# Optimization experiments

Hardware: AMD Instinct MI355X
Metric: run time of the kernel (lower is better)

The kernel has to match this reference:

```python
import jax, jax.numpy as jnp
import numpy as np

N_NODES = 100_000
N_EDGES = 1_000_000
IN_CH = 32
EDGE_CH = 16
OUT_CH = 32
D_CAT = 2 * IN_CH + EDGE_CH  # 80
D_MID = 56                   # linspace(80, 32, 3)[1]


def setup_inputs() -> dict:
    key = jax.random.key(0)
    ks = jax.random.split(key, 8)
    x = jax.random.normal(ks[0], (N_NODES, IN_CH), dtype=jnp.float32)
    edge_index = jax.random.randint(ks[1], (2, N_EDGES), 0, N_NODES, dtype=jnp.int64)
    edge_attr = jax.random.normal(ks[2], (N_EDGES, EDGE_CH), dtype=jnp.float32)
    # MLP params: Linear(80->56), Linear(56->32), bias=True (homogeneous_flag=False)
    W1 = jax.random.normal(ks[3], (D_CAT, D_MID), dtype=jnp.float32) / np.sqrt(D_CAT).astype(np.float32)
    b1 = jnp.zeros((D_MID,), dtype=jnp.float32)
    W2 = jax.random.normal(ks[4], (D_MID, OUT_CH), dtype=jnp.float32) / np.sqrt(D_MID).astype(np.float32)
    b2 = jnp.zeros((OUT_CH,), dtype=jnp.float32)
    return {"x": x, "edge_index": edge_index, "edge_attr": edge_attr,
            "W1": W1, "b1": b1, "W2": W2, "b2": b2}


def reference(x, edge_index, edge_attr, W1, b1, W2, b2):
    num_nodes = x.shape[0]
    rol, col = edge_index[0], edge_index[1]
    # gather node pairs + concat edge features: [E, 2*in + edge]
    e = jnp.concatenate([x[rol], x[col], edge_attr], axis=-1)
    # edge MLP (LeakyReLU after every layer, as in IterGNN's MLP)
    h = jax.nn.leaky_relu(e @ W1 + b1)
    v = jax.nn.leaky_relu(h @ W2 + b2)  # [E, out]
    # Max aggregation by destination node (scatter-max); empty segments -> 0
    agg = jax.ops.segment_max(v, col, num_segments=num_nodes)
    agg = jnp.where(jnp.isneginf(agg), jnp.zeros((), dtype=agg.dtype), agg)
    # elementwise max with trailing slice of input features
    out = jnp.maximum(agg, x[:, -v.shape[-1]:])
    return out
```

## Files before the change

### kernel.cpp

```cpp
#include <hip/hip_runtime.h>

#define N_NODES 100000
#define IN_CH 32
#define EDGE_CH 16
#define OUT_CH 32
#define D_CAT 80
#define D_MID 56

#define BKT_SHIFT 6
#define BKT_NODES 64
#define NB 1563
#define NB_ALL 1568
#define CAP 1024

#define NSUP 196
#define CAP_SUP 5632
#define K1_EDGES 4096
#define K2_ITERS 11

#define EPB 128
#define W1F_SH 6144
#define W2F_SH 2048
#define WIMG_SH (W1F_SH + W2F_SH)
#define FEATF_SH 12288
#define HF_SH 8192

#define AGG_LD 33
#define ENC_NEGINF 0x007FFFFFu

typedef short short8 __attribute__((ext_vector_type(8)));
typedef float f32x4 __attribute__((ext_vector_type(4)));
typedef int i32x2 __attribute__((ext_vector_type(2)));

#define WS_IMG    0
#define WS_B1     16384
#define WS_B2     16640
#define WS_SUPCNT 16768
#define WS_GCNT   17664
#define WS_SUPREC 24576
#define WS_REC    8855552
#define WS_XB_A   21700608
#define XB_BYTES  6400000
#define WS_NEED_A ((size_t)WS_XB_A)
#define WS_NEED_AX ((size_t)WS_XB_A + XB_BYTES)
#define WS_XB_B   12869632
#define WS_NEED_B ((size_t)WS_XB_B)
#define WS_NEED_BX ((size_t)WS_XB_B + XB_BYTES)

__device__ __forceinline__ unsigned fenc(float f) {
    unsigned u = __float_as_uint(f);
    return (u & 0x80000000u) ? ~u : (u | 0x80000000u);
}
__device__ __forceinline__ float fdec(unsigned u) {
    u = (u & 0x80000000u) ? (u ^ 0x80000000u) : ~u;
    return __uint_as_float(u);
}
__device__ __forceinline__ float bfr(float f) {
    unsigned u = __float_as_uint(f);
    u = (u + 0x7FFFu + ((u >> 16) & 1u)) & 0xFFFF0000u;
    return __uint_as_float(u);
}
__device__ __forceinline__ unsigned short bf16b(float f) {
    unsigned u = __float_as_uint(f);
    return (unsigned short)((u + 0x7FFFu + ((u >> 16) & 1u)) >> 16);
}

__device__ __forceinline__ void convert_x_bf16(const float* __restrict__ x,
                                               unsigned short* __restrict__ xb,
                                               int gtid, int gstride) {
    const int tot = N_NODES * IN_CH / 8;
    for (int i = gtid; i < tot; i += gstride) {
        float4 a = ((const float4*)x)[2 * i];
        float4 b = ((const float4*)x)[2 * i + 1];
        short8 p = { (short)bf16b(a.x), (short)bf16b(a.y), (short)bf16b(a.z), (short)bf16b(a.w),
                     (short)bf16b(b.x), (short)bf16b(b.y), (short)bf16b(b.z), (short)bf16b(b.w) };
        *(short8*)&xb[i * 8] = p;
    }
}

__device__ void build_weight_image(const float* __restrict__ W1, const float* __restrict__ b1,
                                   const float* __restrict__ W2, const float* __restrict__ b2,
                                   unsigned short* __restrict__ wsImg,
                                   float* __restrict__ wsb1, float* __restrict__ wsb2,
                                   int t, int nthr) {
    for (int s = t; s < W1F_SH; s += nthr) {
        int j = s & 7, l = (s >> 3) & 63, fi = s >> 9;
        int nt = fi & 3, ks = fi >> 2;
        int l15 = l & 15, quad = l >> 4;
        int n = nt * 16 + l15, k = ks * 32 + quad * 8 + j;
        wsImg[s] = (n < D_MID && k < D_CAT) ? bf16b(W1[k * D_MID + n]) : (unsigned short)0;
    }
    for (int s = t; s < W2F_SH; s += nthr) {
        int j = s & 7, l = (s >> 3) & 63, fi = s >> 9;
        int nt = fi & 1, ks = fi >> 1;
        int l15 = l & 15, quad = l >> 4;
        int n = nt * 16 + l15, k = ks * 32 + quad * 8 + j;
        wsImg[W1F_SH + s] = (k < D_MID) ? bf16b(W2[k * OUT_CH + n]) : (unsigned short)0;
    }
    if (t < 64) wsb1[t] = (t < D_MID) ? bfr(b1[t]) : 0.f;
    else if (t < 96) wsb2[t - 64] = bfr(b2[t - 64]);
}

__global__ __launch_bounds__(512) void coarse_bin(
    const int* __restrict__ ei, int nE, int* __restrict__ gSupCnt, int2* __restrict__ supRec,
    const float* __restrict__ W1, const float* __restrict__ b1,
    const float* __restrict__ W2, const float* __restrict__ b2,
    unsigned short* __restrict__ wsImg, float* __restrict__ wsb1, float* __restrict__ wsb2)
{
    __shared__ int2 staged[K1_EDGES];
    __shared__ int cnt[256], sc[256], cur[256], wb[256];
    const int t = threadIdx.x;
    if (blockIdx.x == 0) build_weight_image(W1, b1, W2, b2, wsImg, wsb1, wsb2, t, 512);
    if (t < 256) cnt[t] = 0;
    __syncthreads();

    const int lo = blockIdx.x * K1_EDGES;
    int rdst[8], rsrc[8];
#pragma unroll
    for (int k = 0; k < 8; ++k) {
        int e = lo + k * 512 + t;
        bool v = e < nE;
        rdst[k] = v ? __builtin_nontemporal_load(ei + nE + e) : -1;
        rsrc[k] = v ? __builtin_nontemporal_load(ei + e) : 0;
        if ((unsigned)rdst[k] >= N_NODES) rdst[k] = -1;
        if ((unsigned)rsrc[k] >= N_NODES) rsrc[k] = 0;
        if (rdst[k] >= 0) atomicAdd(&cnt[rdst[k] >> 9], 1);
    }
    __syncthreads();
    if (t < 256) sc[t] = cnt[t];
    __syncthreads();
    for (int off = 1; off < 256; off <<= 1) {
        int v = 0;
        if (t < 256 && t >= off) v = sc[t - off];
        __syncthreads();
        if (t < 256) sc[t] += v;
        __syncthreads();
    }
    if (t < NSUP) {
        int c = cnt[t];
        int excl = sc[t] - c;
        int g = c ? atomicAdd(&gSupCnt[t], c) : 0;
        wb[t] = t * CAP_SUP + g - excl;
        cur[t] = excl;
    }
    __syncthreads();
#pragma unroll
    for (int k = 0; k < 8; ++k) {
        if (rdst[k] >= 0) {
            int s = rdst[k] >> 9;
            int pos = atomicAdd(&cur[s], 1);
            int e = lo + k * 512 + t;
            staged[pos] = make_int2(rsrc[k] | (s << 24), ((rdst[k] & 511) << 20) | e);
        }
    }
    __syncthreads();
    int nv = sc[NSUP - 1];
    for (int i = t; i < nv; i += 512) {
        int2 r = staged[i];
        int s = (unsigned)r.x >> 24;
        int addr = wb[s] + i;
        if (addr - s * CAP_SUP < CAP_SUP)
            supRec[addr] = make_int2(r.x & 0x00FFFFFF, r.y);
    }
}

__global__ __launch_bounds__(512) void fine_bin(
    const int* __restrict__ gSupCnt, const int2* __restrict__ supRec,
    int* __restrict__ gCnt, int2* __restrict__ rec,
    const float* __restrict__ x, unsigned short* __restrict__ xb)
{
    __shared__ int cur8[8];
    const int s = blockIdx.x, t = threadIdx.x;
    const int lane = t & 63;

    if (xb) convert_x_bf16(x, xb, s * 512 + t, NSUP * 512);

    const int cntS = min(gSupCnt[s], CAP_SUP);
    if (t < 8) cur8[t] = 0;
    __syncthreads();

    int2 r[K2_ITERS];
#pragma unroll
    for (int k = 0; k < K2_ITERS; ++k) {
        int i = k * 512 + t;
        r[k] = (i < cntS) ? supRec[(size_t)s * CAP_SUP + i] : make_int2(0, 0);
    }
#pragma unroll
    for (int k = 0; k < K2_ITERS; ++k) {
        int i = k * 512 + t;
        bool v = i < cntS;
        int f = v ? ((r[k].y >> 26) & 7) : -1;
        int rank = 0, wbase = 0;
#pragma unroll
        for (int vv = 0; vv < 8; ++vv) {
            unsigned long long m = __ballot(f == vv);
            if (lane == vv) wbase = m ? atomicAdd(&cur8[vv], (int)__popcll(m)) : 0;
            if (f == vv) rank = (int)__popcll(m & ((1ull << lane) - 1ull));
        }
        int base = __shfl(wbase, f & 7);
        if (v) {
            int pos = base + rank;
            if (pos < CAP)
                rec[(size_t)(s * 8 + f) * CAP + pos] =
                    make_int2(r[k].x, (((r[k].y >> 20) & 63) << 20) | (r[k].y & 0xFFFFF));
        }
    }
    __syncthreads();
    if (t < 8) gCnt[s * 8 + t] = min(cur8[t], CAP);
}

__global__ __launch_bounds__(512) void scatter_append(
    const int* __restrict__ ei, int* __restrict__ gCnt, int2* __restrict__ rec, int nE,
    const float* __restrict__ W1, const float* __restrict__ b1,
    const float* __restrict__ W2, const float* __restrict__ b2,
    unsigned short* __restrict__ wsImg, float* __restrict__ wsb1, float* __restrict__ wsb2,
    const float* __restrict__ x, unsigned short* __restrict__ xb)
{
    __shared__ int lh[NB];
    __shared__ int lbase[NB];
    if (blockIdx.x == 0) build_weight_image(W1, b1, W2, b2, wsImg, wsb1, wsb2, threadIdx.x, 512);
    if (xb) convert_x_bf16(x, xb, blockIdx.x * 512 + threadIdx.x, gridDim.x * 512);
    for (int i = threadIdx.x; i < NB; i += 512) lh[i] = 0;
    __syncthreads();
    int per = (nE + gridDim.x - 1) / gridDim.x;
    int lo = blockIdx.x * per;
    int hi = min(lo + per, nE);
    for (int e = lo + threadIdx.x; e < hi; e += 512) {
        int dst = __builtin_nontemporal_load(ei + nE + e);
        if ((unsigned)dst < N_NODES) atomicAdd(&lh[dst >> BKT_SHIFT], 1);
    }
    __syncthreads();
    for (int i = threadIdx.x; i < NB; i += 512) {
        int c = lh[i];
        lbase[i] = c ? atomicAdd(&gCnt[i], c) : 0;
        lh[i] = 0;
    }
    __syncthreads();
    for (int e = lo + threadIdx.x; e < hi; e += 512) {
        int dst = __builtin_nontemporal_load(ei + nE + e);
        if ((unsigned)dst >= N_NODES) continue;
        int b = dst >> BKT_SHIFT;
        int p = lbase[b] + atomicAdd(&lh[b], 1);
        if (p >= CAP) continue;
        int src = __builtin_nontemporal_load(ei + e);
        if ((unsigned)src >= N_NODES) src = 0;
        rec[(size_t)b * CAP + p] = make_int2(src, ((dst & (BKT_NODES - 1)) << 20) | e);
    }
}

template<int XB>
__global__ __launch_bounds__(512, 6) void bucket_mlp(
    const float* __restrict__ x, const unsigned short* __restrict__ xb,
    const float* __restrict__ ea,
    const int2* __restrict__ rec, const int* __restrict__ gCnt,
    const unsigned short* __restrict__ wsImg,
    const float* __restrict__ wsb1, const float* __restrict__ wsb2,
    float* __restrict__ out)
{
    __shared__ unsigned short sFeatF[FEATF_SH];
    __shared__ unsigned short sWgt[WIMG_SH];
    __shared__ unsigned aggL[BKT_NODES * AGG_LD];
    __shared__ float sb1f[64];
    __shared__ float sb2f[32];
    __shared__ int sdl[EPB];

    unsigned short* const sW1F = sWgt;
    unsigned short* const sW2F = sWgt + W1F_SH;
    unsigned short* const sHF  = sFeatF;

    const int t = threadIdx.x;
    const int nodeBase = blockIdx.x << BKT_SHIFT;
    const int base = blockIdx.x * CAP;
    const int cnt  = min(gCnt[blockIdx.x], CAP);

    for (int i = t; i < WIMG_SH / 8; i += 512)
        *(short8*)&sWgt[i * 8] = *(const short8*)(wsImg + i * 8);
    for (int i = t; i < BKT_NODES * AGG_LD; i += 512) aggL[i] = ENC_NEGINF;
    if (t < 64) sb1f[t] = wsb1[t];
    else if (t < 96) sb2f[t - 64] = wsb2[t - 64];

    const int wave = t >> 6;
    const int l15  = t & 15;
    const int quad = (t & 63) >> 4;
    const int wm   = wave * 16;
    const int lane = t & 63;
    const int slot = t >> 2, q = t & 3;
    const int sl15 = slot & 15, swave = slot >> 4;

    float4 rv[6];
    short8 rv16[3];
    int rdl;

    auto loadChunk = [&](int c0e) {
        int idx = c0e + slot;
        bool ok = idx < cnt;
        i32x2 r2 = ok ? *(const i32x2*)(rec + base + idx) : (i32x2){0, 0};
        rdl = ok ? ((r2.y >> 20) & 63) : -1;
        int e = r2.y & 0xFFFFF;
        int src = r2.x;
        int dn = nodeBase + ((r2.y >> 20) & 63);
        if constexpr (XB) {
            const short8* xs8 = (const short8*)(xb + (size_t)src * IN_CH);
            const short8* xd8 = (const short8*)(xb + (size_t)dn * IN_CH);
            const float* ep = ea + (size_t)e * EDGE_CH;
#pragma unroll
            for (int k = 0; k < 3; ++k) {
                int cj = 3 * q + k;
                short8 pv = {0, 0, 0, 0, 0, 0, 0, 0};
                if (ok) {
                    if (cj < 4) pv = xs8[cj];
                    else if (cj < 8) pv = xd8[cj - 4];
                    else if (cj < 10) {
                        float4 a = ((const float4*)ep)[(cj - 8) * 2];
                        float4 b = ((const float4*)ep)[(cj - 8) * 2 + 1];
                        pv = short8{ (short)bf16b(a.x), (short)bf16b(a.y), (short)bf16b(a.z), (short)bf16b(a.w),
                                     (short)bf16b(b.x), (short)bf16b(b.y), (short)bf16b(b.z), (short)bf16b(b.w) };
                    }
                }
                rv16[k] = pv;
            }
        } else {
            const float* xs = x + (size_t)src * IN_CH;
            const float* xd = x + (size_t)dn * IN_CH;
            const float* ep = ea + (size_t)e * EDGE_CH;
            float4 z = make_float4(0, 0, 0, 0);
#pragma unroll
            for (int k = 0; k < 3; ++k) {
                int cj = 3 * q + k;
                const float* p = nullptr;
                if (cj < 4) p = xs + cj * 8;
                else if (cj < 8) p = xd + (cj - 4) * 8;
                else if (cj < 10) p = ep + (cj - 8) * 8;
                if (ok && p) { rv[2 * k] = ((const float4*)p)[0]; rv[2 * k + 1] = ((const float4*)p)[1]; }
                else { rv[2 * k] = z; rv[2 * k + 1] = z; }
            }
        }
    };
    auto storeChunk = [&]() {
        if (q == 0) sdl[slot] = rdl;
#pragma unroll
        for (int k = 0; k < 3; ++k) {
            int cj = 3 * q + k;
            short8 p8;
            if constexpr (XB) {
                p8 = rv16[k];
            } else {
                float4 a = rv[2 * k], b = rv[2 * k + 1];
                p8 = short8{ (short)bf16b(a.x), (short)bf16b(a.y), (short)bf16b(a.z), (short)bf16b(a.w),
                             (short)bf16b(b.x), (short)bf16b(b.y), (short)bf16b(b.z), (short)bf16b(b.w) };
            }
            int a16 = (swave * 3 + (cj >> 2)) * 64 + (cj & 3) * 16 + sl15;
            *(short8*)&sFeatF[a16 * 8] = p8;
        }
    };

    loadChunk(0);
    for (int c0e = 0; c0e < cnt; c0e += EPB) {
        storeChunk();
        __syncthreads();
        loadChunk(c0e + EPB);

        f32x4 acc[4];
#pragma unroll
        for (int nt = 0; nt < 4; ++nt) acc[nt] = (f32x4){0.f, 0.f, 0.f, 0.f};
#pragma unroll
        for (int ks = 0; ks < 3; ++ks) {
            short8 bfrag = *(const short8*)&sFeatF[((wave * 3 + ks) * 64 + lane) * 8];
#pragma unroll
            for (int nt = 0; nt < 4; ++nt) {
                short8 afrag = *(const short8*)&sW1F[((ks * 4 + nt) * 64 + lane) * 8];
                acc[nt] = __builtin_amdgcn_mfma_f32_16x16x32_bf16(afrag, bfrag, acc[nt], 0, 0, 0);
            }
        }
        __syncthreads();

        {
#pragma unroll
            for (int nt = 0; nt < 4; ++nt) {
                int c0 = nt * 16 + quad * 4;
                int ks2 = nt >> 1;
                int quad2 = (nt * 2 + (quad >> 1)) & 3;
                int off = (quad & 1) * 4;
                ushort4 p;
#pragma unroll
                for (int j = 0; j < 4; ++j) {
                    float v = acc[nt][j] + sb1f[c0 + j];
                    v = (v > 0.f) ? v : 0.01f * v;
                    ((unsigned short*)&p)[j] = (c0 + j < D_MID) ? bf16b(v) : (unsigned short)0;
                }
                *(ushort4*)&sHF[((wave * 2 + ks2) * 64 + quad2 * 16 + l15) * 8 + off] = p;
            }
        }
        __syncthreads();

        f32x4 acc2[2];
#pragma unroll
        for (int nt = 0; nt < 2; ++nt) acc2[nt] = (f32x4){0.f, 0.f, 0.f, 0.f};
#pragma unroll
        for (int ks = 0; ks < 2; ++ks) {
            short8 bfrag = *(const short8*)&sHF[((wave * 2 + ks) * 64 + lane) * 8];
#pragma unroll
            for (int nt = 0; nt < 2; ++nt) {
                short8 afrag = *(const short8*)&sW2F[((ks * 2 + nt) * 64 + lane) * 8];
                acc2[nt] = __builtin_amdgcn_mfma_f32_16x16x32_bf16(afrag, bfrag, acc2[nt], 0, 0, 0);
            }
        }

        {
            int dl = sdl[wm + l15];
            if (dl >= 0) {
                unsigned* arow = &aggL[dl * AGG_LD];
#pragma unroll
                for (int nt = 0; nt < 2; ++nt) {
                    int c0 = nt * 16 + quad * 4;
#pragma unroll
                    for (int j = 0; j < 4; ++j) {
                        float v = acc2[nt][j] + sb2f[c0 + j];
                        v = (v > 0.f) ? v : 0.01f * v;
                        atomicMax(arow + c0 + j, fenc(bfr(v)));
                    }
                }
            }
        }
        __syncthreads();
    }
    __syncthreads();

    {
        int nl = t >> 3, g4 = t & 7;
        int node = nodeBase + nl;
        if (node < N_NODES) {
            const unsigned* ar = &aggL[nl * AGG_LD + g4 * 4];
            float4 o;
            if constexpr (XB) {
                ushort4 xw = ((const ushort4*)(xb + (size_t)node * IN_CH))[g4];
                o.x = fmaxf((ar[0] == ENC_NEGINF) ? 0.f : fdec(ar[0]), __uint_as_float((unsigned)xw.x << 16));
                o.y = fmaxf((ar[1] == ENC_NEGINF) ? 0.f : fdec(ar[1]), __uint_as_float((unsigned)xw.y << 16));
                o.z = fmaxf((ar[2] == ENC_NEGINF) ? 0.f : fdec(ar[2]), __uint_as_float((unsigned)xw.z << 16));
                o.w = fmaxf((ar[3] == ENC_NEGINF) ? 0.f : fdec(ar[3]), __uint_as_float((unsigned)xw.w << 16));
            } else {
                float4 xv = ((const float4*)(x + (size_t)node * IN_CH))[g4];
                o.x = fmaxf((ar[0] == ENC_NEGINF) ? 0.f : fdec(ar[0]), bfr(xv.x));
                o.y = fmaxf((ar[1] == ENC_NEGINF) ? 0.f : fdec(ar[1]), bfr(xv.y));
                o.z = fmaxf((ar[2] == ENC_NEGINF) ? 0.f : fdec(ar[2]), bfr(xv.z));
                o.w = fmaxf((ar[3] == ENC_NEGINF) ? 0.f : fdec(ar[3]), bfr(xv.w));
            }
            ((float4*)(out + (size_t)node * OUT_CH))[g4] = o;
        }
    }
}

extern "C" void kernel_launch(void* const* d_in, const int* in_sizes, int n_in,
                              void* d_out, int out_size, void* d_ws, size_t ws_size,
                              hipStream_t stream) {
    const float* x  = (const float*)d_in[0];
    const int*   ei = (const int*)d_in[1];
    const float* ea = (const float*)d_in[2];
    const float* W1 = (const float*)d_in[3];
    const float* b1 = (const float*)d_in[4];
    const float* W2 = (const float*)d_in[5];
    const float* b2 = (const float*)d_in[6];

    char* ws = (char*)d_ws;
    unsigned short* wsImg = (unsigned short*)(ws + WS_IMG);
    float* wsb1 = (float*)(ws + WS_B1);
    float* wsb2 = (float*)(ws + WS_B2);
    int* gSupCnt = (int*)(ws + WS_SUPCNT);
    int* gCnt = (int*)(ws + WS_GCNT);

    const int nE = in_sizes[1] / 2;
    float* out = (float*)d_out;

    if (ws_size >= WS_NEED_A) {
        int2* supRec = (int2*)(ws + WS_SUPREC);
        int2* rec    = (int2*)(ws + WS_REC);
        bool xbOn = ws_size >= WS_NEED_AX;
        unsigned short* xb = xbOn ? (unsigned short*)(ws + WS_XB_A) : nullptr;
        hipMemsetAsync(gSupCnt, 0, NSUP * sizeof(int), stream);
        coarse_bin<<<(nE + K1_EDGES - 1) / K1_EDGES, 512, 0, stream>>>(
            ei, nE, gSupCnt, supRec, W1, b1, W2, b2, wsImg, wsb1, wsb2);
        fine_bin<<<NSUP, 512, 0, stream>>>(gSupCnt, supRec, gCnt, rec, x, xb);
        if (xbOn)
            bucket_mlp<1><<<NB, 512, 0, stream>>>(x, xb, ea, rec, gCnt, wsImg, wsb1, wsb2, out);
        else
            bucket_mlp<0><<<NB, 512, 0, stream>>>(x, nullptr, ea, rec, gCnt, wsImg, wsb1, wsb2, out);
    } else {
        int2* rec = (int2*)(ws + 24576);
        bool xbOn = ws_size >= WS_NEED_BX;
        unsigned short* xb = xbOn ? (unsigned short*)(ws + WS_XB_B) : nullptr;
        hipMemsetAsync(gCnt, 0, NB_ALL * sizeof(int), stream);
        scatter_append<<<128, 512, 0, stream>>>(ei, gCnt, rec, nE, W1, b1, W2, b2,
                                                wsImg, wsb1, wsb2, x, xb);
        if (xbOn)
            bucket_mlp<1><<<NB, 512, 0, stream>>>(x, xb, ea, rec, gCnt, wsImg, wsb1, wsb2, out);
        else
            bucket_mlp<0><<<NB, 512, 0, stream>>>(x, nullptr, ea, rec, gCnt, wsImg, wsb1, wsb2, out);
    }
}
```

Baseline: 227.2 us.

## Precompute per-destination-node W1 contribution once per bucket and double edge tile size

Splits the first MLP layer so the x[dst] part (plus bias) is computed once per destination node in the bucket via MFMA and stored in shared memory. Per-edge work then only gathers x[src] and edge_attr (K=48 padded to 64 instead of 80 padded to 96). This removes the per-edge gather of destination features and a third of the layer-1 MFMAs. Edges per iteration go from 128 to 256 with two tiles per wave, and the record prefetch is pipelined one chunk further ahead. Occupancy drops from 6 to 4 blocks per CU to fit the extra registers and shared memory. Adding the fp32 destination partial sum to the edge partial changes bf16 rounding slightly.

```diff
diff --git a/kernel.cpp b/kernel.cpp
--- a/kernel.cpp
+++ b/kernel.cpp
@@ -18,13 +18,16 @@
 #define K1_EDGES 4096
 #define K2_ITERS 11
 
-#define EPB 128
-#define W1F_SH 6144
+#define EPB 256
+#define NT_E 16
+
+#define W1F_SH 4096
 #define W2F_SH 2048
-#define WIMG_SH (W1F_SH + W2F_SH)
-#define FEATF_SH 12288
-#define HF_SH 8192
-
+#define W1D_SH 2048
+#define WIMG_SH (W1F_SH + W2F_SH + W1D_SH)
+#define FEATF_SH (NT_E * 2 * 64 * 8)
+
+#define HSTRIDE 68
 #define AGG_LD 33
 #define ENC_NEGINF 0x007FFFFFu
 
@@ -64,6 +67,10 @@
     unsigned u = __float_as_uint(f);
     return (unsigned short)((u + 0x7FFFu + ((u >> 16) & 1u)) >> 16);
 }
+__device__ __forceinline__ short8 cvt8(float4 a, float4 b) {
+    return short8{ (short)bf16b(a.x), (short)bf16b(a.y), (short)bf16b(a.z), (short)bf16b(a.w),
+                   (short)bf16b(b.x), (short)bf16b(b.y), (short)bf16b(b.z), (short)bf16b(b.w) };
+}
 
 __device__ __forceinline__ void convert_x_bf16(const float* __restrict__ x,
                                                unsigned short* __restrict__ xb,
@@ -72,9 +79,7 @@
     for (int i = gtid; i < tot; i += gstride) {
         float4 a = ((const float4*)x)[2 * i];
         float4 b = ((const float4*)x)[2 * i + 1];
-        short8 p = { (short)bf16b(a.x), (short)bf16b(a.y), (short)bf16b(a.z), (short)bf16b(a.w),
-                     (short)bf16b(b.x), (short)bf16b(b.y), (short)bf16b(b.z), (short)bf16b(b.w) };
-        *(short8*)&xb[i * 8] = p;
+        *(short8*)&xb[i * 8] = cvt8(a, b);
     }
 }
 
@@ -86,16 +91,25 @@
     for (int s = t; s < W1F_SH; s += nthr) {
         int j = s & 7, l = (s >> 3) & 63, fi = s >> 9;
         int nt = fi & 3, ks = fi >> 2;
-        int l15 = l & 15, quad = l >> 4;
-        int n = nt * 16 + l15, k = ks * 32 + quad * 8 + j;
-        wsImg[s] = (n < D_MID && k < D_CAT) ? bf16b(W1[k * D_MID + n]) : (unsigned short)0;
+        int n = nt * 16 + (l & 15), kl = ks * 32 + (l >> 4) * 8 + j;
+        unsigned short v = 0;
+        if (n < D_MID) {
+            if (kl < 32) v = bf16b(W1[kl * D_MID + n]);
+            else if (kl < 48) v = bf16b(W1[(64 + kl - 32) * D_MID + n]);
+        }
+        wsImg[s] = v;
     }
     for (int s = t; s < W2F_SH; s += nthr) {
         int j = s & 7, l = (s >> 3) & 63, fi = s >> 9;
         int nt = fi & 1, ks = fi >> 1;
-        int l15 = l & 15, quad = l >> 4;
-        int n = nt * 16 + l15, k = ks * 32 + quad * 8 + j;
-        wsImg[W1F_SH + s] = (k < D_MID) ? bf16b(W2[k * OUT_CH + n]) : (unsigned short)0;
+        int n = nt * 16 + (l & 15), kl = ks * 32 + (l >> 4) * 8 + j;
+        wsImg[W1F_SH + s] = (kl < D_MID) ? bf16b(W2[kl * OUT_CH + n]) : (unsigned short)0;
+    }
+    for (int s = t; s < W1D_SH; s += nthr) {
+        int j = s & 7, l = (s >> 3) & 63, fi = s >> 9;
+        int nt = fi & 3;
+        int n = nt * 16 + (l & 15), kl = (l >> 4) * 8 + j;
+        wsImg[W1F_SH + W2F_SH + s] = (n < D_MID) ? bf16b(W1[(32 + kl) * D_MID + n]) : (unsigned short)0;
     }
     if (t < 64) wsb1[t] = (t < D_MID) ? bfr(b1[t]) : 0.f;
     else if (t < 96) wsb2[t - 64] = bfr(b2[t - 64]);
@@ -249,7 +263,7 @@
 }
 
 template<int XB>
-__global__ __launch_bounds__(512, 6) void bucket_mlp(
+__global__ __launch_bounds__(512, 4) void bucket_mlp(
     const float* __restrict__ x, const unsigned short* __restrict__ xb,
     const float* __restrict__ ea,
     const int2* __restrict__ rec, const int* __restrict__ gCnt,
@@ -259,6 +273,7 @@
 {
     __shared__ unsigned short sFeatF[FEATF_SH];
     __shared__ unsigned short sWgt[WIMG_SH];
+    __shared__ float sHdst[BKT_NODES * HSTRIDE];
     __shared__ unsigned aggL[BKT_NODES * AGG_LD];
     __shared__ float sb1f[64];
     __shared__ float sb2f[32];
@@ -266,6 +281,7 @@
 
     unsigned short* const sW1F = sWgt;
     unsigned short* const sW2F = sWgt + W1F_SH;
+    unsigned short* const sW1D = sWgt + W1F_SH + W2F_SH;
     unsigned short* const sHF  = sFeatF;
 
     const int t = threadIdx.x;
@@ -282,132 +298,155 @@
     const int wave = t >> 6;
     const int l15  = t & 15;
     const int quad = (t & 63) >> 4;
-    const int wm   = wave * 16;
     const int lane = t & 63;
-    const int slot = t >> 2, q = t & 3;
-    const int sl15 = slot & 15, swave = slot >> 4;
-
-    float4 rv[6];
-    short8 rv16[3];
+    const int slot = t >> 1, q = t & 1;
+    const int sl15 = slot & 15, set = slot >> 4;
+
+    short8 rv16[4];
     int rdl;
 
-    auto loadChunk = [&](int c0e) {
-        int idx = c0e + slot;
-        bool ok = idx < cnt;
-        i32x2 r2 = ok ? *(const i32x2*)(rec + base + idx) : (i32x2){0, 0};
+    auto loadRec = [&](int idx) -> i32x2 {
+        return (idx < cnt) ? *(const i32x2*)(rec + base + idx) : (i32x2){0, 0};
+    };
+    auto gather = [&](i32x2 r2, bool ok) {
         rdl = ok ? ((r2.y >> 20) & 63) : -1;
-        int e = r2.y & 0xFFFFF;
-        int src = r2.x;
-        int dn = nodeBase + ((r2.y >> 20) & 63);
-        if constexpr (XB) {
-            const short8* xs8 = (const short8*)(xb + (size_t)src * IN_CH);
-            const short8* xd8 = (const short8*)(xb + (size_t)dn * IN_CH);
-            const float* ep = ea + (size_t)e * EDGE_CH;
-#pragma unroll
-            for (int k = 0; k < 3; ++k) {
-                int cj = 3 * q + k;
-                short8 pv = {0, 0, 0, 0, 0, 0, 0, 0};
-                if (ok) {
-                    if (cj < 4) pv = xs8[cj];
-                    else if (cj < 8) pv = xd8[cj - 4];
-                    else if (cj < 10) {
-                        float4 a = ((const float4*)ep)[(cj - 8) * 2];
-                        float4 b = ((const float4*)ep)[(cj - 8) * 2 + 1];
-                        pv = short8{ (short)bf16b(a.x), (short)bf16b(a.y), (short)bf16b(a.z), (short)bf16b(a.w),
-                                     (short)bf16b(b.x), (short)bf16b(b.y), (short)bf16b(b.z), (short)bf16b(b.w) };
-                    }
-                }
-                rv16[k] = pv;
+        short8 z = {0, 0, 0, 0, 0, 0, 0, 0};
+        if (q == 0) {
+            if constexpr (XB) {
+                const short8* xs8 = (const short8*)(xb + (size_t)r2.x * IN_CH);
+#pragma unroll
+                for (int k = 0; k < 4; ++k) rv16[k] = ok ? xs8[k] : z;
+            } else {
+                const float* xs = x + (size_t)r2.x * IN_CH;
+#pragma unroll
+                for (int k = 0; k < 4; ++k)
+                    rv16[k] = ok ? cvt8(((const float4*)xs)[2 * k], ((const float4*)xs)[2 * k + 1]) : z;
             }
         } else {
-            const float* xs = x + (size_t)src * IN_CH;
-            const float* xd = x + (size_t)dn * IN_CH;
-            const float* ep = ea + (size_t)e * EDGE_CH;
-            float4 z = make_float4(0, 0, 0, 0);
-#pragma unroll
-            for (int k = 0; k < 3; ++k) {
-                int cj = 3 * q + k;
-                const float* p = nullptr;
-                if (cj < 4) p = xs + cj * 8;
-                else if (cj < 8) p = xd + (cj - 4) * 8;
-                else if (cj < 10) p = ep + (cj - 8) * 8;
-                if (ok && p) { rv[2 * k] = ((const float4*)p)[0]; rv[2 * k + 1] = ((const float4*)p)[1]; }
-                else { rv[2 * k] = z; rv[2 * k + 1] = z; }
-            }
+            const float* ep = ea + (size_t)(r2.y & 0xFFFFF) * EDGE_CH;
+#pragma unroll
+            for (int k = 0; k < 2; ++k)
+                rv16[k] = ok ? cvt8(((const float4*)ep)[2 * k], ((const float4*)ep)[2 * k + 1]) : z;
+            rv16[2] = z; rv16[3] = z;
         }
     };
     auto storeChunk = [&]() {
         if (q == 0) sdl[slot] = rdl;
 #pragma unroll
-        for (int k = 0; k < 3; ++k) {
-            int cj = 3 * q + k;
-            short8 p8;
+        for (int k = 0; k < 4; ++k) {
+            int cj = q * 4 + k;
+            int a16 = (set * 2 + (cj >> 2)) * 64 + (cj & 3) * 16 + sl15;
+            *(short8*)&sFeatF[a16 * 8] = rv16[k];
+        }
+    };
+
+    i32x2 recC = loadRec(slot);
+    i32x2 recN = loadRec(EPB + slot);
+    gather(recC, slot < cnt);
+
+    __syncthreads();
+
+    {
+        const int ntile = wave & 3, mh = wave >> 2;
+        int node = nodeBase + ntile * 16 + l15;
+        short8 bfr8 = {0, 0, 0, 0, 0, 0, 0, 0};
+        if (node < N_NODES) {
             if constexpr (XB) {
-                p8 = rv16[k];
+                bfr8 = *(const short8*)(xb + (size_t)node * IN_CH + quad * 8);
             } else {
-                float4 a = rv[2 * k], b = rv[2 * k + 1];
-                p8 = short8{ (short)bf16b(a.x), (short)bf16b(a.y), (short)bf16b(a.z), (short)bf16b(a.w),
-                             (short)bf16b(b.x), (short)bf16b(b.y), (short)bf16b(b.z), (short)bf16b(b.w) };
-            }
-            int a16 = (swave * 3 + (cj >> 2)) * 64 + (cj & 3) * 16 + sl15;
-            *(short8*)&sFeatF[a16 * 8] = p8;
-        }
-    };
-
-    loadChunk(0);
+                const float* xp = x + (size_t)node * IN_CH + quad * 8;
+                bfr8 = cvt8(((const float4*)xp)[0], ((const float4*)xp)[1]);
+            }
+        }
+        f32x4 accd[2] = {(f32x4){0.f, 0.f, 0.f, 0.f}, (f32x4){0.f, 0.f, 0.f, 0.f}};
+#pragma unroll
+        for (int i = 0; i < 2; ++i) {
+            int nt = mh * 2 + i;
+            short8 af = *(const short8*)&sW1D[(nt * 64 + lane) * 8];
+            accd[i] = __builtin_amdgcn_mfma_f32_16x16x32_bf16(af, bfr8, accd[i], 0, 0, 0);
+        }
+#pragma unroll
+        for (int i = 0; i < 2; ++i) {
+            int nt = mh * 2 + i, c0 = nt * 16 + quad * 4;
+            float4 vv;
+#pragma unroll
+            for (int j = 0; j < 4; ++j) {
+                int c = c0 + j;
+                ((float*)&vv)[j] = (c < D_MID) ? accd[i][j] + sb1f[c] : 0.f;
+            }
+            *(float4*)&sHdst[(ntile * 16 + l15) * HSTRIDE + c0] = vv;
+        }
+    }
+
     for (int c0e = 0; c0e < cnt; c0e += EPB) {
         storeChunk();
         __syncthreads();
-        loadChunk(c0e + EPB);
-
-        f32x4 acc[4];
-#pragma unroll
-        for (int nt = 0; nt < 4; ++nt) acc[nt] = (f32x4){0.f, 0.f, 0.f, 0.f};
-#pragma unroll
-        for (int ks = 0; ks < 3; ++ks) {
-            short8 bfrag = *(const short8*)&sFeatF[((wave * 3 + ks) * 64 + lane) * 8];
+        gather(recN, (c0e + EPB + slot) < cnt);
+        recN = loadRec(c0e + 2 * EPB + slot);
+
+        f32x4 acc[2][4];
+#pragma unroll
+        for (int ei = 0; ei < 2; ++ei)
+#pragma unroll
+            for (int nt = 0; nt < 4; ++nt) acc[ei][nt] = (f32x4){0.f, 0.f, 0.f, 0.f};
+#pragma unroll
+        for (int ks = 0; ks < 2; ++ks) {
+            short8 bf0 = *(const short8*)&sFeatF[((wave * 2 + ks) * 64 + lane) * 8];
+            short8 bf1 = *(const short8*)&sFeatF[(((wave + 8) * 2 + ks) * 64 + lane) * 8];
 #pragma unroll
             for (int nt = 0; nt < 4; ++nt) {
-                short8 afrag = *(const short8*)&sW1F[((ks * 4 + nt) * 64 + lane) * 8];
-                acc[nt] = __builtin_amdgcn_mfma_f32_16x16x32_bf16(afrag, bfrag, acc[nt], 0, 0, 0);
+                short8 af = *(const short8*)&sW1F[((ks * 4 + nt) * 64 + lane) * 8];
+                acc[0][nt] = __builtin_amdgcn_mfma_f32_16x16x32_bf16(af, bf0, acc[0][nt], 0, 0, 0);
+                acc[1][nt] = __builtin_amdgcn_mfma_f32_16x16x32_bf16(af, bf1, acc[1][nt], 0, 0, 0);
             }
         }
         __syncthreads();
 
-        {
+#pragma unroll
+        for (int ei = 0; ei < 2; ++ei) {
+            int et = wave + ei * 8;
+            int dl = sdl[et * 16 + l15];
+            const float* hrow = &sHdst[((dl >= 0) ? dl : 0) * HSTRIDE];
 #pragma unroll
             for (int nt = 0; nt < 4; ++nt) {
                 int c0 = nt * 16 + quad * 4;
+                float4 hd = *(const float4*)&hrow[c0];
                 int ks2 = nt >> 1;
                 int quad2 = (nt * 2 + (quad >> 1)) & 3;
                 int off = (quad & 1) * 4;
                 ushort4 p;
 #pragma unroll
                 for (int j = 0; j < 4; ++j) {
-                    float v = acc[nt][j] + sb1f[c0 + j];
+                    float v = acc[ei][nt][j] + ((const float*)&hd)[j];
                     v = (v > 0.f) ? v : 0.01f * v;
                     ((unsigned short*)&p)[j] = (c0 + j < D_MID) ? bf16b(v) : (unsigned short)0;
                 }
-                *(ushort4*)&sHF[((wave * 2 + ks2) * 64 + quad2 * 16 + l15) * 8 + off] = p;
+                *(ushort4*)&sHF[((et * 2 + ks2) * 64 + quad2 * 16 + l15) * 8 + off] = p;
             }
         }
         __syncthreads();
 
-        f32x4 acc2[2];
-#pragma unroll
-        for (int nt = 0; nt < 2; ++nt) acc2[nt] = (f32x4){0.f, 0.f, 0.f, 0.f};
+        f32x4 acc2[2][2];
+#pragma unroll
+        for (int ei = 0; ei < 2; ++ei)
+#pragma unroll
+            for (int nt = 0; nt < 2; ++nt) acc2[ei][nt] = (f32x4){0.f, 0.f, 0.f, 0.f};
 #pragma unroll
         for (int ks = 0; ks < 2; ++ks) {
-            short8 bfrag = *(const short8*)&sHF[((wave * 2 + ks) * 64 + lane) * 8];
+            short8 bf0 = *(const short8*)&sHF[((wave * 2 + ks) * 64 + lane) * 8];
+            short8 bf1 = *(const short8*)&sHF[(((wave + 8) * 2 + ks) * 64 + lane) * 8];
 #pragma unroll
             for (int nt = 0; nt < 2; ++nt) {
-                short8 afrag = *(const short8*)&sW2F[((ks * 2 + nt) * 64 + lane) * 8];
-                acc2[nt] = __builtin_amdgcn_mfma_f32_16x16x32_bf16(afrag, bfrag, acc2[nt], 0, 0, 0);
-            }
-        }
-
-        {
-            int dl = sdl[wm + l15];
+                short8 af = *(const short8*)&sW2F[((ks * 2 + nt) * 64 + lane) * 8];
+                acc2[0][nt] = __builtin_amdgcn_mfma_f32_16x16x32_bf16(af, bf0, acc2[0][nt], 0, 0, 0);
+                acc2[1][nt] = __builtin_amdgcn_mfma_f32_16x16x32_bf16(af, bf1, acc2[1][nt], 0, 0, 0);
+            }
+        }
+
+#pragma unroll
+        for (int ei = 0; ei < 2; ++ei) {
+            int et = wave + ei * 8;
+            int dl = sdl[et * 16 + l15];
             if (dl >= 0) {
                 unsigned* arow = &aggL[dl * AGG_LD];
 #pragma unroll
@@ -415,7 +454,7 @@
                     int c0 = nt * 16 + quad * 4;
 #pragma unroll
                     for (int j = 0; j < 4; ++j) {
-                        float v = acc2[nt][j] + sb2f[c0 + j];
+                        float v = acc2[ei][nt][j] + sb2f[c0 + j];
                         v = (v > 0.f) ? v : 0.01f * v;
                         atomicMax(arow + c0 + j, fenc(bfr(v)));
                     }
```

Result: faster. 208.5 us (-8.2%).
